# Performance work log

Hardware: AMD Instinct MI355X
Metric: run time of the kernel (lower is better)

## Reference

```python
import jax, jax.numpy as jnp
import numpy as np

EPS = 1e-6
ROPE_THETA = 1000000.0

def _rmsnorm(x, scale):
    var = jnp.mean(jnp.square(x), axis=-1, keepdims=True)
    return x * jax.lax.rsqrt(var + EPS) * scale

def _rope(x, positions):
    # x: [B, h, T, H]; GPT-NeoX style rotate-half
    H = x.shape[-1]
    half = H // 2
    inv_freq = 1.0 / (ROPE_THETA ** (jnp.arange(half, dtype=jnp.float32) * 2.0 / H))
    ang = positions.astype(jnp.float32)[:, None] * inv_freq[None, :]  # [T, half]
    cos, sin = jnp.cos(ang), jnp.sin(ang)
    x1, x2 = x[..., :half], x[..., half:]
    return jnp.concatenate([x1 * cos - x2 * sin, x2 * cos + x1 * sin], axis=-1)

def setup_inputs() -> dict:
    key = jax.random.key(0)
    ks = jax.random.split(key, 16)
    B, T, D = 2, 2048, 2048
    N, K, H = 16, 2, 128
    I = 5504
    s = 0.02
    return {
        "x": jax.random.normal(ks[0], (B, T, D), jnp.float32),
        "positions": jnp.arange(T, dtype=jnp.int32),
        "ln1_scale": jnp.ones((D,), jnp.float32),
        "q_w": jax.random.normal(ks[1], (N, D, H), jnp.float32) * s,
        "q_b": jax.random.normal(ks[2], (N, H), jnp.float32) * s,
        "k_w": jax.random.normal(ks[3], (K, D, H), jnp.float32) * s,
        "k_b": jax.random.normal(ks[4], (K, H), jnp.float32) * s,
        "v_w": jax.random.normal(ks[5], (K, D, H), jnp.float32) * s,
        "v_b": jax.random.normal(ks[6], (K, H), jnp.float32) * s,
        "o_w": jax.random.normal(ks[7], (N, H, D), jnp.float32) * s,
        "ln2_scale": jnp.ones((D,), jnp.float32),
        "gate_w": jax.random.normal(ks[8], (D, I), jnp.float32) * s,
        "up_w": jax.random.normal(ks[9], (D, I), jnp.float32) * s,
        "down_w": jax.random.normal(ks[10], (I, D), jnp.float32) * s,
    }

def reference(x, positions, ln1_scale, q_w, q_b, k_w, k_b, v_w, v_b, o_w,
              ln2_scale, gate_w, up_w, down_w):
    B, T, D = x.shape
    N, _, H = q_w.shape
    K = k_w.shape[0]
    group = N // K

    h = _rmsnorm(x, ln1_scale)

    # Projections (per source einsums) + bias
    q = jnp.einsum('btd,ndh->bnth', h, q_w) + q_b[None, :, None, :]
    k = jnp.einsum('btd,kdh->bkth', h, k_w) + k_b[None, :, None, :]
    v = jnp.einsum('btd,kdh->bkth', h, v_w) + v_b[None, :, None, :]

    q = _rope(q, positions) * (H ** -0.5)
    k = _rope(k, positions)

    # GQA: expand kv heads to query heads
    k = jnp.repeat(k, group, axis=1)  # [B,N,T,H]
    v = jnp.repeat(v, group, axis=1)

    # Causal self-attention (prefill path: kv cache filled from k, v)
    scores = jnp.einsum('bnth,bnsh->bnts', q, k)
    causal = positions[:, None] >= positions[None, :]  # [T, T]
    scores = jnp.where(causal[None, None, :, :], scores, -jnp.inf)
    probs = jax.nn.softmax(scores, axis=-1)
    attn = jnp.einsum('bnts,bnsh->bnth', probs, v)

    o = jnp.einsum('bnth,nhd->btd', attn, o_w)

    # Residual + post-attn norm + SwiGLU MLP + residual
    res = o + x
    h2 = _rmsnorm(res, ln2_scale)
    fuse = jax.nn.silu(h2 @ gate_w) * (h2 @ up_w)
    return res + fuse @ down_w
```

## Files before the change

kernel.cpp:

```cpp
#include <hip/hip_runtime.h>
#include <cstdint>
#include <cstddef>

typedef unsigned short u16;
typedef __attribute__((ext_vector_type(8))) short short8;
typedef __attribute__((ext_vector_type(4))) float f32x4;

#define DEV __device__ __forceinline__

DEV float bf2f(u16 v) { union { unsigned u; float f; } x; x.u = ((unsigned)v) << 16; return x.f; }
DEV u16 f2bf(float f) {
  union { float f; unsigned u; } x; x.f = f;
  unsigned r = x.u + 0x7fffu + ((x.u >> 16) & 1u);
  return (u16)(r >> 16);
}

DEV void gload_lds16(const void* g, void* l) {
  __builtin_amdgcn_global_load_lds((const __attribute__((address_space(1))) void*)g,
                                   (__attribute__((address_space(3))) void*)l, 16, 0, 0);
}

#define BARRIER __builtin_amdgcn_s_barrier()
#define VM0 asm volatile("s_waitcnt vmcnt(0)" ::: "memory")
#define VM4 asm volatile("s_waitcnt vmcnt(4)" ::: "memory")

DEV void rmsnorm_row(const float* __restrict__ x, const float* __restrict__ scale,
                     u16* __restrict__ out, int row, int tid, float* red)
{
  const float* xr = x + (size_t)row * 2048;
  const float4 v0 = *(const float4*)&xr[tid * 8];
  const float4 v1 = *(const float4*)&xr[tid * 8 + 4];
  float ss = v0.x * v0.x + v0.y * v0.y + v0.z * v0.z + v0.w * v0.w +
             v1.x * v1.x + v1.y * v1.y + v1.z * v1.z + v1.w * v1.w;
#pragma unroll
  for (int d = 32; d > 0; d >>= 1) ss += __shfl_down(ss, d);
  if ((tid & 63) == 0) red[tid >> 6] = ss;
  __syncthreads();
  const float tot = red[0] + red[1] + red[2] + red[3];
  const float inv = rsqrtf(tot * (1.f / 2048.f) + 1e-6f);
  const float* sc = scale + tid * 8;
  short8 ov;
  ov[0] = (short)f2bf(v0.x * inv * sc[0]); ov[1] = (short)f2bf(v0.y * inv * sc[1]);
  ov[2] = (short)f2bf(v0.z * inv * sc[2]); ov[3] = (short)f2bf(v0.w * inv * sc[3]);
  ov[4] = (short)f2bf(v1.x * inv * sc[4]); ov[5] = (short)f2bf(v1.y * inv * sc[5]);
  ov[6] = (short)f2bf(v1.z * inv * sc[6]); ov[7] = (short)f2bf(v1.w * inv * sc[7]);
  *(short8*)&out[(size_t)row * 2048 + tid * 8] = ov;
}

DEV void transpose_tile(const float* __restrict__ in, u16* __restrict__ out,
                        int R, int C, int mode, int bx, int by, int bz,
                        int tid, float (&tile)[64][65])
{
  const int tx = tid & 31, ty = tid >> 5;
  const int c0 = bx * 64, r0 = by * 64;
  const float* inb = in + (size_t)bz * R * C;
  u16* outb = out + (size_t)bz * R * C;
#pragma unroll
  for (int i = 0; i < 8; ++i) {
    const int r = ty + i * 8;
    const float2 v = *(const float2*)&inb[(size_t)(r0 + r) * C + c0 + tx * 2];
    tile[r][tx * 2] = v.x;
    tile[r][tx * 2 + 1] = v.y;
  }
  __syncthreads();
#pragma unroll
  for (int i = 0; i < 8; ++i) {
    const int jj = ty + i * 8;
    const int j = c0 + jj;
    const int prow = mode ? ((j >> 7) * 256 + (((j >> 5) & 3) << 6) + ((mode == 2) << 5) + (j & 31))
                          : j;
    const unsigned a = f2bf(tile[tx * 2][jj]);
    const unsigned b = f2bf(tile[tx * 2 + 1][jj]);
    *(unsigned*)&outb[(size_t)prow * R + r0 + tx * 2] = a | (b << 16);
  }
}

__global__ __launch_bounds__(256) void prep_kernel(
    const float* __restrict__ q_w, const float* __restrict__ k_w,
    const float* __restrict__ v_w, const float* __restrict__ o_w,
    const float* __restrict__ qb, const float* __restrict__ kb,
    const float* __restrict__ vb,
    const float* __restrict__ x, const float* __restrict__ ln1,
    u16* __restrict__ wqkv_t, u16* __restrict__ o_wt,
    float* __restrict__ bias, u16* __restrict__ hbuf)
{
  __shared__ float tile[64][65];
  const int bid = (int)blockIdx.x;
  const int tid = threadIdx.x;
  if (bid < 1024) {
    transpose_tile(q_w, wqkv_t, 2048, 128, 0, bid & 1, (bid >> 1) & 31, bid >> 6, tid, tile);
  } else if (bid < 1152) {
    const int l = bid - 1024;
    transpose_tile(k_w, wqkv_t + 2048LL * 2048, 2048, 128, 0, l & 1, (l >> 1) & 31, l >> 6, tid, tile);
  } else if (bid < 1280) {
    const int l = bid - 1152;
    transpose_tile(v_w, wqkv_t + 2304LL * 2048, 2048, 128, 0, l & 1, (l >> 1) & 31, l >> 6, tid, tile);
  } else if (bid < 2304) {
    const int l = bid - 1280;
    transpose_tile(o_w, o_wt, 2048, 2048, 0, l & 31, l >> 5, 0, tid, tile);
  } else if (bid < 2314) {
    const int i = (bid - 2304) * 256 + tid;
    if (i < 2048) bias[i] = qb[i];
    else if (i < 2304) bias[i] = kb[i - 2048];
    else if (i < 2560) bias[i] = vb[i - 2304];
  } else {
    rmsnorm_row(x, ln1, hbuf, bid - 2314, tid, &tile[0][0]);
  }
}

__global__ __launch_bounds__(256) void rmsnorm_kernel(
    const float* __restrict__ x, const float* __restrict__ scale, u16* __restrict__ out)
{
  __shared__ float red[4];
  rmsnorm_row(x, scale, out, blockIdx.x, threadIdx.x, red);
}

__global__ __launch_bounds__(256, 2) void qkv_prep2_kernel(
    const u16* __restrict__ A, const u16* __restrict__ Bt,
    u16* __restrict__ C, const float* __restrict__ aux,
    const float* __restrict__ gate_w, const float* __restrict__ up_w,
    const float* __restrict__ down_w,
    u16* __restrict__ gu_t, u16* __restrict__ d_t)
{
  constexpr int BM = 128, BN = 128, TB = 256, GR = 8;
  constexpr int MFRAG = 4, AISS = 4, BISS = 4, WN = 2;
  constexpr int NGEMM = 640;
  const int N = 2560, K = 2048, lda = 2048, ldb = 2048;
  __shared__ __align__(16) u16 As[2][BM * 64];
  __shared__ __align__(16) u16 Bs[3][BN * 64];

  const int tid = threadIdx.x;
  const int bid = (int)blockIdx.x;

  if (bid >= NGEMM) {
    auto& tile = *reinterpret_cast<float(*)[64][65]>(&As[0][0]);
    const int l = bid - NGEMM;
    if (l < 2752) {
      transpose_tile(gate_w, gu_t, 2048, 5504, 1, l % 86, l / 86, 0, tid, tile);
    } else if (l < 5504) {
      const int m = l - 2752;
      transpose_tile(up_w, gu_t, 2048, 5504, 2, m % 86, m / 86, 0, tid, tile);
    } else {
      const int m = l - 5504;
      transpose_tile(down_w, d_t, 5504, 2048, 0, m & 31, m >> 5, 0, tid, tile);
    }
    return;
  }

  const int wv = tid >> 6, lane = tid & 63, lo = lane & 15, hi = lane >> 4;
  const int wm = wv / WN, wn = wv % WN;

  const int id = (bid & 7) * (NGEMM >> 3) + (bid >> 3);
  const int ncol = N / BN;
  const int rg = id % GR, cc = (id / GR) % ncol, gg = id / (GR * ncol);
  const int by = gg * GR + rg, bx = cc;
  const int row0 = by * BM, col0 = bx * BN;

  const f32x4 fz = {0.f, 0.f, 0.f, 0.f};
  f32x4 acc[MFRAG][4];
#pragma unroll
  for (int m = 0; m < MFRAG; ++m)
#pragma unroll
    for (int n = 0; n < 4; ++n) acc[m][n] = fz;

  const int nt = K >> 6;

  auto STAGE_A = [&](int kt, int ab) {
#pragma unroll
    for (int i = 0; i < AISS; ++i) {
      const int f = i * TB + tid;
      const int rp = f >> 3, sp = tid & 7;
      gload_lds16(A + (size_t)(row0 + rp) * lda + kt * 64 + ((sp ^ (rp & 7)) * 8),
                  (char*)&As[ab][0] + (i * TB + wv * 64) * 16);
    }
  };
  auto STAGE_B = [&](int kt, int bb) {
#pragma unroll
    for (int i = 0; i < BISS; ++i) {
      const int f = i * TB + tid;
      const int rp = f >> 3, sp = tid & 7;
      gload_lds16(Bt + (size_t)(col0 + rp) * ldb + kt * 64 + ((sp ^ (rp & 7)) * 8),
                  (char*)&Bs[bb][0] + (i * TB + wv * 64) * 16);
    }
  };

#define LDA8Q(ARR, BUF, S, G)                                                    \
  _Pragma("unroll")                                                              \
  for (int mt = 0; mt < 4; ++mt) {                                               \
    const int r = wm * (BM / 2) + ((G) * 4 + mt) * 16 + lo;                      \
    ARR[mt] = *(const short8*)&As[BUF][r * 64 + (((S) * 4 + hi) ^ (r & 7)) * 8]; \
  }
#define LDB8Q(ARR, BUF, S)                                                       \
  _Pragma("unroll")                                                              \
  for (int nn = 0; nn < 4; ++nn) {                                               \
    const int r = wn * 64 + nn * 16 + lo;                                        \
    ARR[nn] = *(const short8*)&Bs[BUF][r * 64 + (((S) * 4 + hi) ^ (r & 7)) * 8]; \
  }
#define MFMA16Q(AR, BR, G)                                                       \
  __builtin_amdgcn_s_setprio(1);                                                 \
  _Pragma("unroll")                                                              \
  for (int mt = 0; mt < 4; ++mt)                                                 \
    _Pragma("unroll")                                                            \
    for (int nn = 0; nn < 4; ++nn)                                               \
      acc[(G) * 4 + mt][nn] = __builtin_amdgcn_mfma_f32_16x16x32_bf16(           \
          AR[mt], BR[nn], acc[(G) * 4 + mt][nn], 0, 0, 0);                       \
  __builtin_amdgcn_s_setprio(0);

  STAGE_A(0, 0); STAGE_B(0, 0); STAGE_B(1, 1);
  VM4; BARRIER;

  int ab = 0, bcur = 0;
  for (int t = 0; t < nt; ++t) {
    const bool preA = (t + 1 < nt);
    const bool preB = (t + 2 < nt);
    const int bs2 = (bcur >= 1) ? bcur - 1 : 2;
    short8 a0[4], b0[4], a1[4], b1[4];
    LDA8Q(a0, ab, 0, 0); LDB8Q(b0, bcur, 0);
    LDA8Q(a1, ab, 1, 0); LDB8Q(b1, bcur, 1);
    if (preA) STAGE_A(t + 1, ab ^ 1);
    if (preB) STAGE_B(t + 2, bs2);
    MFMA16Q(a0, b0, 0);
    MFMA16Q(a1, b1, 0);
    if (preA) { if (preB) VM4; else VM0; }
    BARRIER;
    ab ^= 1;
    bcur = (bcur == 2) ? 0 : bcur + 1;
  }
#undef LDA8Q
#undef LDB8Q
#undef MFMA16Q

#pragma unroll
  for (int fm = 0; fm < MFRAG; ++fm) {
#pragma unroll
    for (int nn = 0; nn < 4; ++nn) {
      const int col = col0 + wn * 64 + nn * 16 + lo;
#pragma unroll
      for (int j = 0; j < 4; ++j) {
        const int row = row0 + wm * (BM / 2) + fm * 16 + hi * 4 + j;
        C[(size_t)row * N + col] = f2bf(acc[fm][nn][j] + aux[col]);
      }
    }
  }
}

template <int BM, int BN, int TB, int MODE, int GR>
__global__ __launch_bounds__(TB, 512 / TB) void gemm_conv_kernel(
    const u16* __restrict__ A, const u16* __restrict__ Bt,
    void* C, const float* __restrict__ aux, int N, int K, int lda, int ldb)
{
  constexpr int MFRAG = BM / 32;
  constexpr int AISS = BM * 8 / TB;
  constexpr int BISS = BN * 8 / TB;
  constexpr int WN = BN / 64;
  __shared__ __align__(16) u16 As[2][BM * 64];
  __shared__ __align__(16) u16 Bs[3][BN * 64];

  const int tid = threadIdx.x;
  const int wv = tid >> 6, lane = tid & 63, lo = lane & 15, hi = lane >> 4;
  const int wm = wv / WN, wn = wv % WN;

  const int nwg = (int)gridDim.x;
  const int id0 = (int)blockIdx.x;
  const int id = (id0 & 7) * (nwg >> 3) + (id0 >> 3);
  const int ncol = N / BN;
  const int rg = id % GR, cc = (id / GR) % ncol, gg = id / (GR * ncol);
  const int by = gg * GR + rg, bx = cc;
  const int row0 = by * BM, col0 = bx * BN;

  const f32x4 fz = {0.f, 0.f, 0.f, 0.f};
  f32x4 acc[MFRAG][4];
#pragma unroll
  for (int m = 0; m < MFRAG; ++m)
#pragma unroll
    for (int n = 0; n < 4; ++n) acc[m][n] = fz;

  const int nt = K >> 6;

  auto STAGE_A = [&](int kt, int ab) {
#pragma unroll
    for (int i = 0; i < AISS; ++i) {
      const int f = i * TB + tid;
      const int rp = f >> 3, sp = tid & 7;
      gload_lds16(A + (size_t)(row0 + rp) * lda + kt * 64 + ((sp ^ (rp & 7)) * 8),
                  (char*)&As[ab][0] + (i * TB + wv * 64) * 16);
    }
  };
  auto STAGE_B = [&](int kt, int bb) {
#pragma unroll
    for (int i = 0; i < BISS; ++i) {
      const int f = i * TB + tid;
      const int rp = f >> 3, sp = tid & 7;
      gload_lds16(Bt + (size_t)(col0 + rp) * ldb + kt * 64 + ((sp ^ (rp & 7)) * 8),
                  (char*)&Bs[bb][0] + (i * TB + wv * 64) * 16);
    }
  };

#define LDA8M(ARR, BUF, S, G)                                                    \
  _Pragma("unroll")                                                              \
  for (int mt = 0; mt < 4; ++mt) {                                               \
    const int r = wm * (BM / 2) + ((G) * 4 + mt) * 16 + lo;                      \
    ARR[mt] = *(const short8*)&As[BUF][r * 64 + (((S) * 4 + hi) ^ (r & 7)) * 8]; \
  }
#define LDB8M(ARR, BUF, S)                                                       \
  _Pragma("unroll")                                                              \
  for (int nn = 0; nn < 4; ++nn) {                                               \
    const int r = wn * 64 + nn * 16 + lo;                                        \
    ARR[nn] = *(const short8*)&Bs[BUF][r * 64 + (((S) * 4 + hi) ^ (r & 7)) * 8]; \
  }
#define MFMA16M(AR, BR, G)                                                       \
  __builtin_amdgcn_s_setprio(1);                                                 \
  _Pragma("unroll")                                                              \
  for (int mt = 0; mt < 4; ++mt)                                                 \
    _Pragma("unroll")                                                            \
    for (int nn = 0; nn < 4; ++nn)                                               \
      acc[(G) * 4 + mt][nn] = __builtin_amdgcn_mfma_f32_16x16x32_bf16(           \
          AR[mt], BR[nn], acc[(G) * 4 + mt][nn], 0, 0, 0);                       \
  __builtin_amdgcn_s_setprio(0);

  STAGE_A(0, 0); STAGE_B(0, 0); STAGE_B(1, 1);
  VM4; BARRIER;

  int ab = 0, bcur = 0;
  for (int t = 0; t < nt; ++t) {
    const bool preA = (t + 1 < nt);
    const bool preB = (t + 2 < nt);
    const int bs2 = (bcur >= 1) ? bcur - 1 : 2;
    if constexpr (BM == 256) {
      short8 a0[4], a1[4], b0[4], a2[4], a3[4], b1[4];
      LDA8M(a0, ab, 0, 0); LDA8M(a1, ab, 0, 1); LDB8M(b0, bcur, 0);
      LDA8M(a2, ab, 1, 0); LDA8M(a3, ab, 1, 1); LDB8M(b1, bcur, 1);
      if (preA) STAGE_A(t + 1, ab ^ 1);
      if (preB) STAGE_B(t + 2, bs2);
      MFMA16M(a0, b0, 0); MFMA16M(a1, b0, 1);
      MFMA16M(a2, b1, 0); MFMA16M(a3, b1, 1);
      if (preA) { if (preB) VM4; else VM0; }
      BARRIER;
    } else {
      short8 a0[4], b0[4], a1[4], b1[4];
      LDA8M(a0, ab, 0, 0); LDB8M(b0, bcur, 0);
      LDA8M(a1, ab, 1, 0); LDB8M(b1, bcur, 1);
      if (preA) STAGE_A(t + 1, ab ^ 1);
      if (preB) STAGE_B(t + 2, bs2);
      MFMA16M(a0, b0, 0);
      MFMA16M(a1, b1, 0);
      if (preA) { if (preB) VM4; else VM0; }
      BARRIER;
    }
    ab ^= 1;
    bcur = (bcur == 2) ? 0 : bcur + 1;
  }
#undef LDA8M
#undef LDB8M
#undef MFMA16M

  float* Cf = (float*)C;
  u16* Ch = (u16*)C;
  if constexpr (MODE == 4) {
    const int ldo = N >> 1;
#pragma unroll
    for (int fm = 0; fm < MFRAG; ++fm) {
#pragma unroll
      for (int nn = 0; nn < 2; ++nn) {
        const int fcol = (col0 >> 1) + wn * 32 + nn * 16 + lo;
#pragma unroll
        for (int j = 0; j < 4; ++j) {
          const int row = row0 + wm * (BM / 2) + fm * 16 + hi * 4 + j;
          const float g = acc[fm][nn][j];
          const float u = acc[fm][nn + 2][j];
          const float sg = g / (1.f + __builtin_amdgcn_exp2f(-1.4426950408889634f * g));
          Ch[(size_t)row * ldo + fcol] = f2bf(sg * u);
        }
      }
    }
  } else {
#pragma unroll
    for (int fm = 0; fm < MFRAG; ++fm) {
#pragma unroll
      for (int nn = 0; nn < 4; ++nn) {
        const int col = col0 + wn * 64 + nn * 16 + lo;
#pragma unroll
        for (int j = 0; j < 4; ++j) {
          const int row = row0 + wm * (BM / 2) + fm * 16 + hi * 4 + j;
          const size_t idx = (size_t)row * N + col;
          const float v = acc[fm][nn][j];
          if (MODE == 0) Cf[idx] = v + aux[col];
          else if (MODE == 1) Cf[idx] = v + aux[idx];
          else if (MODE == 2) Ch[idx] = f2bf(v);
          else Ch[idx] = f2bf(v + aux[col]);
        }
      }
    }
  }
}

__global__ __launch_bounds__(256) void rope_qkv_kernel(
    const u16* __restrict__ qkv, const int* __restrict__ pos,
    u16* __restrict__ Qb, u16* __restrict__ Kb, u16* __restrict__ Vt)
{
  const int idx = blockIdx.x * 256 + threadIdx.x;
  const int bt = idx / 1408;
  const int r = idx - bt * 1408;
  const int t = bt & 2047, b = bt >> 11;
  if (r < 1152) {
    const bool isq = r < 1024;
    const int rr = isq ? r : r - 1024;
    const int n = rr >> 6, hp = rr & 63;
    const u16* q = qkv + (size_t)bt * 2560 + (isq ? 0 : 2048) + n * 128 + hp;
    const float x1 = bf2f(q[0]);
    const float x2 = bf2f(q[64]);
    const float inv = exp2f((float)hp * (-19.931568569324174f / 64.f));
    const float ang = (float)pos[t] * inv;
    float s, c;
    sincosf(ang, &s, &c);
    const float sc = isq ? 0.08838834764831845f * 1.4426950408889634f : 1.f;
    const size_t base = isq ? (((size_t)(b * 16 + n) * 2048 + t) * 128 + hp)
                            : (((size_t)(b * 2 + n) * 2048 + t) * 128 + hp);
    u16* outp = isq ? Qb : Kb;
    outp[base] = f2bf((x1 * c - x2 * s) * sc);
    outp[base + 64] = f2bf((x2 * c + x1 * s) * sc);
  } else {
    const int rr = r - 1152;
    const int kh = rr >> 7, hh = rr & 127;
    Vt[((size_t)((b * 2 + kh) * 128 + hh)) * 2048 + t] =
        qkv[(size_t)bt * 2560 + 2304 + kh * 128 + hh];
  }
}

__global__ __launch_bounds__(512) void attn_kernel(
    const u16* __restrict__ Qb, const u16* __restrict__ Kb,
    const u16* __restrict__ Vt, u16* __restrict__ Out)
{
  __shared__ u16 Ks[2][128 * 128];
  __shared__ u16 Vs[2][128 * 128];
  __shared__ u16 Ps[8][16 * 128];
  const int tid = threadIdx.x;
  const int wave = tid >> 6, lane = tid & 63, lo = lane & 15, hi = lane >> 4;
  const int bn = blockIdx.x;
  const int b = bn >> 4, n = bn & 15, kh = n >> 3;

  const f32x4 fz = {0.f, 0.f, 0.f, 0.f};
  const u16* kg = Kb + (size_t)(b * 2 + kh) * 2048 * 128;
  const u16* vg = Vt + (size_t)(b * 2 + kh) * 128 * 2048;

  auto STAGE = [&](int buf, int s0) {
#pragma unroll
    for (int i = 0; i < 4; ++i) {
      const int gk = i * 512 + tid;
      const int rk = gk >> 4, gck = gk & 15;
      gload_lds16(kg + (size_t)(s0 + rk) * 128 + ((gck ^ (rk & 7)) * 8),
                  (char*)&Ks[buf][0] + (i * 512 + wave * 64) * 16);
      gload_lds16(vg + (size_t)rk * 2048 + s0 + ((gck ^ (rk & 7)) * 8),
                  (char*)&Vs[buf][0] + (i * 512 + wave * 64) * 16);
    }
  };

  auto processTile = [&](int q0) {
    const int nblk = q0 / 128 + 1;
    const u16* qptr = Qb + ((size_t)((b * 16 + n) * 2048) + q0 + wave * 16 + lo) * 128;
    short8 qf[4];
#pragma unroll
    for (int kc = 0; kc < 4; ++kc) qf[kc] = *(const short8*)&qptr[kc * 32 + hi * 8];

    float m_r[4], l_r[4];
    f32x4 oacc[8];
#pragma unroll
    for (int j = 0; j < 4; ++j) { m_r[j] = -1e30f; l_r[j] = 0.f; }
#pragma unroll
    for (int ht = 0; ht < 8; ++ht) oacc[ht] = fz;

    __syncthreads();
    STAGE(0, 0);
    __syncthreads();

    int cur = 0;
    for (int sb = 0; sb < nblk; ++sb) {
      const int s0 = sb * 128;
      if (sb + 1 < nblk) STAGE(cur ^ 1, s0 + 128);

      float sall[8][4];
      __builtin_amdgcn_s_setprio(1);
#pragma unroll
      for (int st = 0; st < 8; ++st) {
        f32x4 s = fz;
#pragma unroll
        for (int kc = 0; kc < 4; ++kc) {
          const int row = st * 16 + lo;
          const int cb = (kc * 64 + hi * 16) ^ ((lo & 7) << 4);
          short8 kf = *(const short8*)&Ks[cur][row * 128 + (cb >> 1)];
          s = __builtin_amdgcn_mfma_f32_16x16x32_bf16(qf[kc], kf, s, 0, 0, 0);
        }
#pragma unroll
        for (int j = 0; j < 4; ++j) sall[st][j] = s[j];
      }
      __builtin_amdgcn_s_setprio(0);

      if (s0 + 128 > q0) {
#pragma unroll
        for (int st = 0; st < 8; ++st) {
          const int sg = s0 + st * 16 + lo;
#pragma unroll
          for (int j = 0; j < 4; ++j) {
            const int qg = q0 + wave * 16 + hi * 4 + j;
            if (sg > qg) sall[st][j] = -1e30f;
          }
        }
      }

      float tmax[4];
#pragma unroll
      for (int j = 0; j < 4; ++j) {
        float t = fmaxf(fmaxf(fmaxf(sall[0][j], sall[1][j]), fmaxf(sall[2][j], sall[3][j])),
                        fmaxf(fmaxf(sall[4][j], sall[5][j]), fmaxf(sall[6][j], sall[7][j])));
        t = fmaxf(t, __shfl_xor(t, 1));
        t = fmaxf(t, __shfl_xor(t, 2));
        t = fmaxf(t, __shfl_xor(t, 4));
        t = fmaxf(t, __shfl_xor(t, 8));
        tmax[j] = t;
      }
      const bool defer = __all((tmax[0] - m_r[0] <= 8.f) & (tmax[1] - m_r[1] <= 8.f) &
                               (tmax[2] - m_r[2] <= 8.f) & (tmax[3] - m_r[3] <= 8.f));
      if (!defer) {
        float alpha[4];
#pragma unroll
        for (int j = 0; j < 4; ++j) {
          const float mnew = fmaxf(m_r[j], tmax[j]);
          alpha[j] = __builtin_amdgcn_exp2f(m_r[j] - mnew);
          m_r[j] = mnew;
          l_r[j] *= alpha[j];
        }
#pragma unroll
        for (int ht = 0; ht < 8; ++ht) {
#pragma unroll
          for (int j = 0; j < 4; ++j) oacc[ht][j] *= alpha[j];
        }
      }

      float rsum[4] = {0.f, 0.f, 0.f, 0.f};
#pragma unroll
      for (int st = 0; st < 8; ++st) {
#pragma unroll
        for (int j = 0; j < 4; ++j) {
          const float p = __builtin_amdgcn_exp2f(sall[st][j] - m_r[j]);
          rsum[j] += p;
          const int row = hi * 4 + j;
          const int cbp = (st * 32 + lo * 2) ^ ((row & 7) << 4);
          Ps[wave][row * 128 + (cbp >> 1)] = f2bf(p);
        }
      }
#pragma unroll
      for (int j = 0; j < 4; ++j) {
        float rs = rsum[j];
        rs += __shfl_xor(rs, 1);
        rs += __shfl_xor(rs, 2);
        rs += __shfl_xor(rs, 4);
        rs += __shfl_xor(rs, 8);
        l_r[j] += rs;
      }

      asm volatile("s_waitcnt lgkmcnt(0)" ::: "memory");
      __builtin_amdgcn_sched_barrier(0);

      short8 pf[4];
#pragma unroll
      for (int s = 0; s < 4; ++s) {
        const int pcb = (s * 64 + hi * 16) ^ ((lo & 7) << 4);
        pf[s] = *(const short8*)&Ps[wave][lo * 128 + (pcb >> 1)];
      }
      __builtin_amdgcn_s_setprio(1);
#pragma unroll
      for (int ht = 0; ht < 8; ++ht) {
        const int row = ht * 16 + lo;
#pragma unroll
        for (int s = 0; s < 4; ++s) {
          const int cb = (s * 64 + hi * 16) ^ ((row & 7) << 4);
          const short8 vf = *(const short8*)&Vs[cur][row * 128 + (cb >> 1)];
          oacc[ht] = __builtin_amdgcn_mfma_f32_16x16x32_bf16(pf[s], vf, oacc[ht], 0, 0, 0);
        }
      }
      __builtin_amdgcn_s_setprio(0);

      if (sb + 1 < nblk) __syncthreads();
      cur ^= 1;
    }

#pragma unroll
    for (int j = 0; j < 4; ++j) {
      const float inv = 1.0f / l_r[j];
      const int trow = q0 + wave * 16 + hi * 4 + j;
      const size_t base = ((size_t)(b * 2048 + trow)) * 2048 + n * 128;
#pragma unroll
      for (int ht = 0; ht < 8; ++ht)
        Out[base + ht * 16 + lo] = f2bf(oacc[ht][j] * inv);
    }
  };

  processTile((int)(15 - blockIdx.y) * 128);
  processTile((int)blockIdx.y * 128);
}

extern "C" void kernel_launch(void* const* d_in, const int* in_sizes, int n_in,
                              void* d_out, int out_size, void* d_ws, size_t ws_size,
                              hipStream_t stream)
{
  const float* x      = (const float*)d_in[0];
  const int*   pos    = (const int*)d_in[1];
  const float* ln1    = (const float*)d_in[2];
  const float* q_w    = (const float*)d_in[3];
  const float* q_b    = (const float*)d_in[4];
  const float* k_w    = (const float*)d_in[5];
  const float* k_b    = (const float*)d_in[6];
  const float* v_w    = (const float*)d_in[7];
  const float* v_b    = (const float*)d_in[8];
  const float* o_w    = (const float*)d_in[9];
  const float* ln2    = (const float*)d_in[10];
  const float* gate_w = (const float*)d_in[11];
  const float* up_w   = (const float*)d_in[12];
  const float* down_w = (const float*)d_in[13];
  float* out = (float*)d_out;

  char* w = (char*)d_ws;
  u16* wqkv_t = (u16*)w;       w += 2560LL * 2048 * 2;
  u16* o_wt   = (u16*)w;       w += 2048LL * 2048 * 2;
  u16* gu_t   = (u16*)w;       w += 11008LL * 2048 * 2;
  u16* d_t    = (u16*)w;       w += 2048LL * 5504 * 2;
  u16* hbuf   = (u16*)w;       w += 4096LL * 2048 * 2;
  float* bias_qkv = (float*)w; w += 2560 * 4;
  char* un = w;
  u16*  qkv   = (u16*)un;
  u16*  Qb    = (u16*)(un + 41943040LL);
  u16*  Kb    = (u16*)(un + 41943040LL + 16777216LL);
  u16*  Vt    = (u16*)(un + 41943040LL + 16777216LL + 2097152LL);
  u16*  attnb = (u16*)(un + 41943040LL + 16777216LL + 2097152LL + 2097152LL);
  u16*  fusebuf = (u16*)un;

  prep_kernel<<<6410, 256, 0, stream>>>(q_w, k_w, v_w, o_w, q_b, k_b, v_b,
                                        x, ln1, wqkv_t, o_wt, bias_qkv, hbuf);

  qkv_prep2_kernel<<<8896, 256, 0, stream>>>(hbuf, wqkv_t, qkv, bias_qkv,
                                             gate_w, up_w, down_w, gu_t, d_t);

  rope_qkv_kernel<<<22528, 256, 0, stream>>>(qkv, pos, Qb, Kb, Vt);
  attn_kernel<<<dim3(32, 8), 512, 0, stream>>>(Qb, Kb, Vt, attnb);
  gemm_conv_kernel<128, 128, 256, 1, 8><<<512, 256, 0, stream>>>(attnb, o_wt, out, x, 2048, 2048, 2048, 2048);
  rmsnorm_kernel<<<4096, 256, 0, stream>>>(out, ln2, hbuf);
  gemm_conv_kernel<256, 256, 512, 4, 4><<<688, 512, 0, stream>>>(hbuf, gu_t, fusebuf, nullptr, 11008, 2048, 2048, 2048);
  gemm_conv_kernel<128, 128, 256, 1, 8><<<512, 256, 0, stream>>>(fusebuf, d_t, out, out, 2048, 5504, 5504, 5504);
}
```

Measured before the change: 517.2 us.

## Fuse RoPE and V-transpose into QKV GEMM epilogue; move MLP weight transposes to prep

The QKV projection GEMM now stages its biased fp32 tile in shared memory and applies RoPE/scaling directly, writing Q, K and transposed V. This removes the separate rope kernel and the intermediate bf16 qkv buffer round trip. The MLP weight transposes previously co-scheduled with the QKV GEMM move into the prep kernel, so the GEMM launch is a compact 640 blocks. The trade-offs are less overlap of transpose work with the GEMM and uncoalesced strided stores in the new epilogue.

```diff
diff --git a/kernel.cpp b/kernel.cpp
--- a/kernel.cpp
+++ b/kernel.cpp
@@ -78,11 +78,14 @@
 __global__ __launch_bounds__(256) void prep_kernel(
     const float* __restrict__ q_w, const float* __restrict__ k_w,
     const float* __restrict__ v_w, const float* __restrict__ o_w,
+    const float* __restrict__ gate_w, const float* __restrict__ up_w,
+    const float* __restrict__ down_w,
     const float* __restrict__ qb, const float* __restrict__ kb,
     const float* __restrict__ vb,
     const float* __restrict__ x, const float* __restrict__ ln1,
     u16* __restrict__ wqkv_t, u16* __restrict__ o_wt,
-    float* __restrict__ bias, u16* __restrict__ hbuf)
+    u16* __restrict__ gu_t, u16* __restrict__ d_t, float* __restrict__ bias,
+    u16* __restrict__ hbuf)
 {
   __shared__ float tile[64][65];
   const int bid = (int)blockIdx.x;
@@ -98,13 +101,22 @@
   } else if (bid < 2304) {
     const int l = bid - 1280;
     transpose_tile(o_w, o_wt, 2048, 2048, 0, l & 31, l >> 5, 0, tid, tile);
-  } else if (bid < 2314) {
-    const int i = (bid - 2304) * 256 + tid;
+  } else if (bid < 5056) {
+    const int l = bid - 2304;
+    transpose_tile(gate_w, gu_t, 2048, 5504, 1, l % 86, l / 86, 0, tid, tile);
+  } else if (bid < 7808) {
+    const int l = bid - 5056;
+    transpose_tile(up_w, gu_t, 2048, 5504, 2, l % 86, l / 86, 0, tid, tile);
+  } else if (bid < 10560) {
+    const int l = bid - 7808;
+    transpose_tile(down_w, d_t, 5504, 2048, 0, l & 31, l >> 5, 0, tid, tile);
+  } else if (bid < 10570) {
+    const int i = (bid - 10560) * 256 + tid;
     if (i < 2048) bias[i] = qb[i];
     else if (i < 2304) bias[i] = kb[i - 2048];
     else if (i < 2560) bias[i] = vb[i - 2304];
   } else {
-    rmsnorm_row(x, ln1, hbuf, bid - 2314, tid, &tile[0][0]);
+    rmsnorm_row(x, ln1, hbuf, bid - 10570, tid, &tile[0][0]);
   }
 }
 
@@ -115,38 +127,22 @@
   rmsnorm_row(x, scale, out, blockIdx.x, threadIdx.x, red);
 }
 
-__global__ __launch_bounds__(256, 2) void qkv_prep2_kernel(
+__global__ __launch_bounds__(256, 2) void qkv_rope_kernel(
     const u16* __restrict__ A, const u16* __restrict__ Bt,
-    u16* __restrict__ C, const float* __restrict__ aux,
-    const float* __restrict__ gate_w, const float* __restrict__ up_w,
-    const float* __restrict__ down_w,
-    u16* __restrict__ gu_t, u16* __restrict__ d_t)
+    const float* __restrict__ bias, const int* __restrict__ pos,
+    u16* __restrict__ Qb, u16* __restrict__ Kb, u16* __restrict__ Vt)
 {
   constexpr int BM = 128, BN = 128, TB = 256, GR = 8;
   constexpr int MFRAG = 4, AISS = 4, BISS = 4, WN = 2;
   constexpr int NGEMM = 640;
   const int N = 2560, K = 2048, lda = 2048, ldb = 2048;
-  __shared__ __align__(16) u16 As[2][BM * 64];
-  __shared__ __align__(16) u16 Bs[3][BN * 64];
+  __shared__ __align__(16) char smem[81920];
+  u16 (&As)[2][BM * 64] = *reinterpret_cast<u16(*)[2][BM * 64]>(smem);
+  u16 (&Bs)[3][BN * 64] = *reinterpret_cast<u16(*)[3][BN * 64]>(smem + 32768);
+  float* lt = reinterpret_cast<float*>(smem);
 
   const int tid = threadIdx.x;
   const int bid = (int)blockIdx.x;
-
-  if (bid >= NGEMM) {
-    auto& tile = *reinterpret_cast<float(*)[64][65]>(&As[0][0]);
-    const int l = bid - NGEMM;
-    if (l < 2752) {
-      transpose_tile(gate_w, gu_t, 2048, 5504, 1, l % 86, l / 86, 0, tid, tile);
-    } else if (l < 5504) {
-      const int m = l - 2752;
-      transpose_tile(up_w, gu_t, 2048, 5504, 2, m % 86, m / 86, 0, tid, tile);
-    } else {
-      const int m = l - 5504;
-      transpose_tile(down_w, d_t, 5504, 2048, 0, m & 31, m >> 5, 0, tid, tile);
-    }
-    return;
-  }
-
   const int wv = tid >> 6, lane = tid & 63, lo = lane & 15, hi = lane >> 4;
   const int wm = wv / WN, wn = wv % WN;
 
@@ -230,17 +226,59 @@
 #undef LDB8Q
 #undef MFMA16Q
 
+  __syncthreads();
 #pragma unroll
   for (int fm = 0; fm < MFRAG; ++fm) {
 #pragma unroll
     for (int nn = 0; nn < 4; ++nn) {
-      const int col = col0 + wn * 64 + nn * 16 + lo;
+      const int c = wn * 64 + nn * 16 + lo;
+      const float bv = bias[col0 + c];
 #pragma unroll
       for (int j = 0; j < 4; ++j) {
-        const int row = row0 + wm * (BM / 2) + fm * 16 + hi * 4 + j;
-        C[(size_t)row * N + col] = f2bf(acc[fm][nn][j] + aux[col]);
-      }
-    }
+        const int r = wm * 64 + fm * 16 + hi * 4 + j;
+        lt[r * 130 + c] = acc[fm][nn][j] + bv;
+      }
+    }
+  }
+  __syncthreads();
+
+  const int head = col0 >> 7;
+  const int b = row0 >> 11;
+  const int t0 = row0 & 2047;
+  if (head < 18) {
+    const int rr = tid >> 1;
+    const int hp0 = (tid & 1) * 32;
+    const int t = t0 + rr;
+    const float pv = (float)pos[t];
+    u16* outp;
+    size_t base;
+    float sc;
+    if (head < 16) {
+      outp = Qb; base = ((size_t)(b * 16 + head) * 2048 + t) * 128;
+      sc = 0.08838834764831845f * 1.4426950408889634f;
+    } else {
+      outp = Kb; base = ((size_t)(b * 2 + (head - 16)) * 2048 + t) * 128;
+      sc = 1.f;
+    }
+#pragma unroll 4
+    for (int i = 0; i < 32; ++i) {
+      const int hp = hp0 + i;
+      const float x1 = lt[rr * 130 + hp];
+      const float x2 = lt[rr * 130 + hp + 64];
+      const float invf = exp2f((float)hp * (-19.931568569324174f / 64.f));
+      float sn, cs;
+      sincosf(pv * invf, &sn, &cs);
+      outp[base + hp] = f2bf((x1 * cs - x2 * sn) * sc);
+      outp[base + hp + 64] = f2bf((x2 * cs + x1 * sn) * sc);
+    }
+  } else {
+    const int kh = head - 18;
+    const int hh = tid >> 1;
+    const int tc0 = (tid & 1) * 64;
+    u16* vb = Vt + ((size_t)((b * 2 + kh) * 128 + hh)) * 2048 + t0 + tc0;
+#pragma unroll 8
+    for (int i = 0; i < 64; ++i)
+      vb[i] = f2bf(lt[(tc0 + i) * 130 + hh]);
   }
 }
 
@@ -394,39 +432,6 @@
   }
 }
 
-__global__ __launch_bounds__(256) void rope_qkv_kernel(
-    const u16* __restrict__ qkv, const int* __restrict__ pos,
-    u16* __restrict__ Qb, u16* __restrict__ Kb, u16* __restrict__ Vt)
-{
-  const int idx = blockIdx.x * 256 + threadIdx.x;
-  const int bt = idx / 1408;
-  const int r = idx - bt * 1408;
-  const int t = bt & 2047, b = bt >> 11;
-  if (r < 1152) {
-    const bool isq = r < 1024;
-    const int rr = isq ? r : r - 1024;
-    const int n = rr >> 6, hp = rr & 63;
-    const u16* q = qkv + (size_t)bt * 2560 + (isq ? 0 : 2048) + n * 128 + hp;
-    const float x1 = bf2f(q[0]);
-    const float x2 = bf2f(q[64]);
-    const float inv = exp2f((float)hp * (-19.931568569324174f / 64.f));
-    const float ang = (float)pos[t] * inv;
-    float s, c;
-    sincosf(ang, &s, &c);
-    const float sc = isq ? 0.08838834764831845f * 1.4426950408889634f : 1.f;
-    const size_t base = isq ? (((size_t)(b * 16 + n) * 2048 + t) * 128 + hp)
-                            : (((size_t)(b * 2 + n) * 2048 + t) * 128 + hp);
-    u16* outp = isq ? Qb : Kb;
-    outp[base] = f2bf((x1 * c - x2 * s) * sc);
-    outp[base + 64] = f2bf((x2 * c + x1 * s) * sc);
-  } else {
-    const int rr = r - 1152;
-    const int kh = rr >> 7, hh = rr & 127;
-    Vt[((size_t)((b * 2 + kh) * 128 + hh)) * 2048 + t] =
-        qkv[(size_t)bt * 2560 + 2304 + kh * 128 + hh];
-  }
-}
-
 __global__ __launch_bounds__(512) void attn_kernel(
     const u16* __restrict__ Qb, const u16* __restrict__ Kb,
     const u16* __restrict__ Vt, u16* __restrict__ Out)
@@ -627,20 +632,18 @@
   u16* hbuf   = (u16*)w;       w += 4096LL * 2048 * 2;
   float* bias_qkv = (float*)w; w += 2560 * 4;
   char* un = w;
-  u16*  qkv   = (u16*)un;
   u16*  Qb    = (u16*)(un + 41943040LL);
   u16*  Kb    = (u16*)(un + 41943040LL + 16777216LL);
   u16*  Vt    = (u16*)(un + 41943040LL + 16777216LL + 2097152LL);
   u16*  attnb = (u16*)(un + 41943040LL + 16777216LL + 2097152LL + 2097152LL);
   u16*  fusebuf = (u16*)un;
 
-  prep_kernel<<<6410, 256, 0, stream>>>(q_w, k_w, v_w, o_w, q_b, k_b, v_b,
-                                        x, ln1, wqkv_t, o_wt, bias_qkv, hbuf);
-
-  qkv_prep2_kernel<<<8896, 256, 0, stream>>>(hbuf, wqkv_t, qkv, bias_qkv,
-                                             gate_w, up_w, down_w, gu_t, d_t);
-
-  rope_qkv_kernel<<<22528, 256, 0, stream>>>(qkv, pos, Qb, Kb, Vt);
+  prep_kernel<<<14666, 256, 0, stream>>>(q_w, k_w, v_w, o_w, gate_w, up_w, down_w,
+                                         q_b, k_b, v_b, x, ln1,
+                                         wqkv_t, o_wt, gu_t, d_t, bias_qkv, hbuf);
+
+  qkv_rope_kernel<<<640, 256, 0, stream>>>(hbuf, wqkv_t, bias_qkv, pos, Qb, Kb, Vt);
+
   attn_kernel<<<dim3(32, 8), 512, 0, stream>>>(Qb, Kb, Vt, attnb);
   gemm_conv_kernel<128, 128, 256, 1, 8><<<512, 256, 0, stream>>>(attnb, o_wt, out, x, 2048, 2048, 2048, 2048);
   rmsnorm_kernel<<<4096, 256, 0, stream>>>(out, ln2, hbuf);
```

Measured after the change: 529.6 us. +2.4%, slower.
